# Kernel optimization log

Hardware: AMD Instinct MI355X
Metric: run time of the kernel (lower is better)

## Reference

```python
import jax, jax.numpy as jnp
import numpy as np

B, C, H, W = 8, 512, 32, 32
HEADS = 8
DIM = C // HEADS
EPS = 1e-5


def setup_inputs() -> dict:
    key = jax.random.key(0)
    ks = jax.random.split(key, 7)
    scale = 1.0 / np.sqrt(C)
    return {
        "x": jax.random.normal(ks[0], (B, C, H, W), dtype=jnp.float32),
        "gn_gamma": jnp.ones((C,), dtype=jnp.float32),
        "gn_beta": jnp.zeros((C,), dtype=jnp.float32),
        "w_qkv": jax.random.normal(ks[1], (3 * HEADS * DIM, C), dtype=jnp.float32) * scale,
        "b_qkv": jax.random.normal(ks[2], (3 * HEADS * DIM,), dtype=jnp.float32) * 0.01,
        "w_proj": jax.random.normal(ks[3], (C, HEADS * DIM), dtype=jnp.float32) * scale,
        "b_proj": jax.random.normal(ks[4], (C,), dtype=jnp.float32) * 0.01,
    }


def reference(x, gn_gamma, gn_beta, w_qkv, b_qkv, w_proj, b_proj):
    b, c, h, w = x.shape
    n = h * w
    # GroupNorm with 1 group: normalize over (C,H,W) per sample (biased var)
    mu = jnp.mean(x, axis=(1, 2, 3), keepdims=True)
    var = jnp.var(x, axis=(1, 2, 3), keepdims=True)
    xn = (x - mu) * jax.lax.rsqrt(var + EPS)
    xn = xn * gn_gamma[None, :, None, None] + gn_beta[None, :, None, None]
    # 1x1 conv QKV projection == channel matmul
    qkv = jnp.einsum('bchw,oc->bohw', xn, w_qkv) + b_qkv[None, :, None, None]
    qkv = qkv.reshape(b, 3, HEADS, DIM, n)  # matches view(B,3*heads,dim,N).chunk(3,dim=1)
    q, k, v = qkv[:, 0], qkv[:, 1], qkv[:, 2]  # each (B, heads, dim, N)
    # scale uses full channel count C, as in the source (C ** -0.5)
    dot = jnp.einsum('bhdn,bhdm->bhnm', q, k) * (c ** -0.5)
    attn = jax.nn.softmax(dot, axis=-1)
    vals = jnp.einsum('bhnm,bhdm->bhdn', attn, v)  # (B, heads, dim, N)
    vals = vals.reshape(b, HEADS * DIM, h, w)
    return jnp.einsum('bchw,oc->bohw', vals, w_proj) + b_proj[None, :, None, None]
```

## Files before the change

### kernel.cpp

```cpp
#include <hip/hip_runtime.h>
#include <hip/hip_bf16.h>
#include <math.h>

#define NB 8
#define NC 512
#define NN 1024
#define NHEADS 8
#define EPSV 1e-5f
#define SC2F 0.06376351307f

typedef __attribute__((ext_vector_type(8))) short bf16x8;
typedef __attribute__((ext_vector_type(4))) short bf16x4;
typedef __attribute__((ext_vector_type(4))) float f32x4;
typedef __attribute__((ext_vector_type(16))) float f32x16;

#define MFMA16(a,b,c) __builtin_amdgcn_mfma_f32_16x16x32_bf16(a,b,c,0,0,0)
#define MFMA32(a,b,c) __builtin_amdgcn_mfma_f32_32x32x16_bf16(a,b,c,0,0,0)

static __device__ __forceinline__ short f2bf(float f) {
    __hip_bfloat16 h = __float2bfloat16(f);
    return *reinterpret_cast<short*>(&h);
}

static __device__ __forceinline__ unsigned cvt_pk_bf16(float lo, float hi) {
    unsigned r;
    asm("v_cvt_pk_bf16_f32 %0, %1, %2" : "=v"(r) : "v"(lo), "v"(hi));
    return r;
}

static __device__ __forceinline__ void gload16(const void* g, void* l) {
    __builtin_amdgcn_global_load_lds((const __attribute__((address_space(1))) void*)g,
                                     (__attribute__((address_space(3))) void*)l, 16, 0, 0);
}

#define WS_PART_SUM 0
#define WS_PART_SQ  1024
#define WS_XNT   4096
#define WS_QT    (WS_XNT  + 2097152)
#define WS_KT    (WS_QT   + 2097152)
#define WS_V     (WS_KT   + 2097152)
#define WS_VALST (WS_V    + 2097152)
#define WS_WQB   (WS_VALST+ 2097152)
#define WS_WPB   (WS_WQB  + 393216)

__global__ __launch_bounds__(256) void prep_kernel(const float* __restrict__ x,
                                                   const float* __restrict__ wq,
                                                   const float* __restrict__ wp,
                                                   float* __restrict__ ws) {
    int blk = blockIdx.x;
    int b = blk >> 6;
    int s = blk & 63;
    const float* xb = x + (size_t)b * (NC * NN) + (size_t)s * 8192;
    float sum = 0.f, sq = 0.f;
    for (int i = threadIdx.x; i < 2048; i += 256) {
        float4 v = ((const float4*)xb)[i];
        sum += v.x + v.y + v.z + v.w;
        sq  += v.x*v.x + v.y*v.y + v.z*v.z + v.w*v.w;
    }
    #pragma unroll
    for (int off = 32; off; off >>= 1) {
        sum += __shfl_down(sum, off);
        sq  += __shfl_down(sq,  off);
    }
    __shared__ float s1[4], s2[4];
    int wave = threadIdx.x >> 6, lane = threadIdx.x & 63;
    if (lane == 0) { s1[wave] = sum; s2[wave] = sq; }

    #pragma unroll
    for (int r = 0; r < 2; r++) {
        int i = blk * 512 + threadIdx.x * 2 + r;
        const float* src;
        __hip_bfloat16* d;
        if (i < 196608) { src = wq; d = (__hip_bfloat16*)(ws + WS_WQB); }
        else            { src = wp; d = (__hip_bfloat16*)(ws + WS_WPB); i -= 196608; }
        float4 v = ((const float4*)src)[i];
        bf16x4 w;
        w[0] = f2bf(v.x); w[1] = f2bf(v.y); w[2] = f2bf(v.z); w[3] = f2bf(v.w);
        *(bf16x4*)(d + (size_t)i*4) = w;
    }

    __syncthreads();
    if (threadIdx.x == 0) {
        float a = 0.f, c2 = 0.f;
        #pragma unroll
        for (int w = 0; w < 4; w++) { a += s1[w]; c2 += s2[w]; }
        ws[WS_PART_SUM + b*64 + s] = a;
        ws[WS_PART_SQ  + b*64 + s] = c2;
    }
}

__global__ __launch_bounds__(256) void normalize_t(const float* __restrict__ x,
                                                   const float* __restrict__ gamma,
                                                   const float* __restrict__ beta,
                                                   const float* __restrict__ ws,
                                                   __hip_bfloat16* __restrict__ xnT) {
    int nt = blockIdx.x & 15, ct = (blockIdx.x >> 4) & 7, b = blockIdx.x >> 7;
    __shared__ __hip_bfloat16 tb[64][72];
    float s = 0.f, q = 0.f;
    const float4* ps = (const float4*)(ws + WS_PART_SUM + b*64);
    const float4* pq = (const float4*)(ws + WS_PART_SQ  + b*64);
    #pragma unroll
    for (int i = 0; i < 16; i++) {
        float4 a = ps[i]; s += a.x + a.y + a.z + a.w;
        float4 c = pq[i]; q += c.x + c.y + c.z + c.w;
    }
    const float inv = 1.f / (float)(NC * NN);
    float mu   = s * inv;
    float var  = q * inv - mu * mu;
    float rstd = rsqrtf(var + EPSV);

    const float* xb = x + ((size_t)b*512 + ct*64)*1024 + nt*64;
    int t = threadIdx.x;
    int cl = t >> 4, n4 = (t & 15) * 4;
    #pragma unroll
    for (int i = 0; i < 4; i++) {
        int c = i*16 + cl;
        float gm = gamma[ct*64 + c];
        float g = gm * rstd;
        float be = beta[ct*64 + c] - mu * g;
        float4 v = *(const float4*)(xb + (size_t)c*1024 + n4);
        tb[n4+0][c] = __float2bfloat16(v.x*g + be);
        tb[n4+1][c] = __float2bfloat16(v.y*g + be);
        tb[n4+2][c] = __float2bfloat16(v.z*g + be);
        tb[n4+3][c] = __float2bfloat16(v.w*g + be);
    }
    __syncthreads();
    #pragma unroll
    for (int i = 0; i < 2; i++) {
        int idx = i*256 + t;
        int n = idx >> 3, c8 = (idx & 7) * 8;
        *(bf16x8*)(xnT + ((size_t)b*1024 + nt*64 + n)*512 + ct*64 + c8) =
            *(const bf16x8*)&tb[n][c8];
    }
}

template<int OT, int MODE>
__global__ __launch_bounds__(256) void gemm_mfma(const __hip_bfloat16* __restrict__ Aw,
                                                 const __hip_bfloat16* __restrict__ Bx,
                                                 const float* __restrict__ bias,
                                                 float* __restrict__ Yout,
                                                 __hip_bfloat16* __restrict__ QTx,
                                                 __hip_bfloat16* __restrict__ KTx,
                                                 __hip_bfloat16* __restrict__ Vx) {
    __shared__ __align__(16) __hip_bfloat16 lds_raw[17408];
    const int bx = blockIdx.x;
    const int swz = (bx & 7) * (OT * 8) + (bx >> 3);
    const int nt = swz & 7;
    const int ot = (swz >> 3) % OT;
    const int bb = swz / (8 * OT);
    const int o0 = ot * 128, n0 = nt * 128;

    const int t = threadIdx.x, wv = t >> 6, l = t & 63;
    const int lr = l & 31, lh = l >> 5;
    const int wr = wv >> 1, wc = wv & 1;

    const __hip_bfloat16* Ag = Aw + (size_t)o0 * 512;
    const __hip_bfloat16* Bg = Bx + ((size_t)bb * 1024 + n0) * 512;
    __hip_bfloat16* Ab = lds_raw;
    __hip_bfloat16* Bb = lds_raw + 128*64;

    f32x16 acc[2][2];
    #pragma unroll
    for (int a1 = 0; a1 < 2; a1++)
        #pragma unroll
        for (int a2 = 0; a2 < 2; a2++)
            #pragma unroll
            for (int r = 0; r < 16; r++) acc[a1][a2][r] = 0.f;

    const int srow = wv*8 + (l >> 3);
    const int sblk = (l & 7) ^ (l >> 3);

    for (int k0 = 0; k0 < 512; k0 += 64) {
        __syncthreads();
        #pragma unroll
        for (int c = 0; c < 4; c++) {
            int row = c*32 + srow;
            gload16(Ag + (size_t)row*512 + k0 + sblk*8, Ab + (c*32 + wv*8)*64);
            gload16(Bg + (size_t)row*512 + k0 + sblk*8, Bb + (c*32 + wv*8)*64);
        }
        __syncthreads();
        #pragma unroll
        for (int ks = 0; ks < 4; ks++) {
            bf16x8 af[2], bfr[2];
            #pragma unroll
            for (int mi = 0; mi < 2; mi++) {
                int row = wr*64 + mi*32 + lr;
                af[mi] = *(const bf16x8*)(Ab + row*64 + (((ks*2 + lh) ^ (row & 7)) * 8));
            }
            #pragma unroll
            for (int ni = 0; ni < 2; ni++) {
                int row = wc*64 + ni*32 + lr;
                bfr[ni] = *(const bf16x8*)(Bb + row*64 + (((ks*2 + lh) ^ (row & 7)) * 8));
            }
            acc[0][0] = MFMA32(af[0], bfr[0], acc[0][0]);
            acc[0][1] = MFMA32(af[0], bfr[1], acc[0][1]);
            acc[1][0] = MFMA32(af[1], bfr[0], acc[1][0]);
            acc[1][1] = MFMA32(af[1], bfr[1], acc[1][1]);
        }
    }

    if (MODE == 0) {
        #pragma unroll
        for (int mi = 0; mi < 2; mi++)
            #pragma unroll
            for (int q = 0; q < 4; q++) {
                int obase = o0 + wr*64 + mi*32 + 8*q + 4*lh;
                float4 bv = *(const float4*)(bias + obase);
                #pragma unroll
                for (int ni = 0; ni < 2; ni++) {
                    int nn = n0 + wc*64 + ni*32 + lr;
                    #pragma unroll
                    for (int j = 0; j < 4; j++)
                        Yout[((size_t)bb*512 + obase + j)*1024 + nn] = acc[mi][ni][q*4+j] + bv[j];
                }
            }
    } else {
        int sec = o0 >> 9;
        if (sec == 2) {
            int od0 = o0 & 511;
            int mperm = ((lr & 12) << 1) + ((lr & 16) >> 2) + (lr & 3);
            #pragma unroll
            for (int mi = 0; mi < 2; mi++)
                #pragma unroll
                for (int q = 0; q < 4; q++) {
                    int ob = wr*64 + mi*32 + 8*q + 4*lh;
                    float4 bv = *(const float4*)(bias + o0 + ob);
                    #pragma unroll
                    for (int j = 0; j < 4; j++) {
                        int ol = od0 + ob + j;
                        int h = ol >> 6, d = ol & 63;
                        __hip_bfloat16* dst = Vx + ((size_t)((bb<<3) + h)*64 + d)*1024;
                        #pragma unroll
                        for (int ni = 0; ni < 2; ni++) {
                            int nn = n0 + wc*64 + ni*32 + mperm;
                            dst[nn] = __float2bfloat16(acc[mi][ni][q*4+j] + bv[j]);
                        }
                    }
                }
        } else {
            const float qs = (sec == 0) ? SC2F : 1.0f;
            __syncthreads();
            __hip_bfloat16* tb = lds_raw;
            #pragma unroll
            for (int mi = 0; mi < 2; mi++)
                #pragma unroll
                for (int q = 0; q < 4; q++) {
                    int ob = wr*64 + mi*32 + 8*q + 4*lh;
                    float4 bv = *(const float4*)(bias + o0 + ob);
                    #pragma unroll
                    for (int ni = 0; ni < 2; ni++) {
                        int nn = wc*64 + ni*32 + lr;
                        bf16x4 w;
                        #pragma unroll
                        for (int j = 0; j < 4; j++) w[j] = f2bf((acc[mi][ni][q*4+j] + bv[j]) * qs);
                        *(bf16x4*)&tb[(size_t)nn*136 + ob] = w;
                    }
                }
            __syncthreads();
            __hip_bfloat16* dst0 = (sec == 0) ? QTx : KTx;
            int h0 = (o0 & 511) >> 6;
            #pragma unroll
            for (int i = 0; i < 8; i++) {
                int idx = i*256 + t;
                int n = idx >> 4, rem = idx & 15;
                int hh = rem >> 3, slot = rem & 7;
                int hf32 = (slot & 4) << 3;
                int g4   = (slot & 3) << 2;
                bf16x4 lo = *(const bf16x4*)&tb[(size_t)n*136 + hh*64 + hf32 + g4];
                bf16x4 hi = *(const bf16x4*)&tb[(size_t)n*136 + hh*64 + hf32 + 16 + g4];
                bf16x8 w;
                w[0]=lo[0]; w[1]=lo[1]; w[2]=lo[2]; w[3]=lo[3];
                w[4]=hi[0]; w[5]=hi[1]; w[6]=hi[2]; w[7]=hi[3];
                *(bf16x8*)(dst0 + ((size_t)((bb<<3) + h0 + hh)*1024 + n0 + n)*64 + slot*8) = w;
            }
        }
    }
}

__global__ __launch_bounds__(512) void attn_mfma(const __hip_bfloat16* __restrict__ QT,
                                                 const __hip_bfloat16* __restrict__ KT,
                                                 const __hip_bfloat16* __restrict__ Vb,
                                                 __hip_bfloat16* __restrict__ valsT) {
    const int bh = ((blockIdx.x & 7) << 3) | ((blockIdx.x >> 3) & 7);
    const int qt = blockIdx.x >> 6;
    const int t = threadIdx.x;
    const int wv = t >> 6, lane = t & 63;
    const int g = lane >> 4, li = lane & 15;

    const __hip_bfloat16* QTg = QT + (size_t)bh * NN * 64;
    const __hip_bfloat16* KTg = KT + (size_t)bh * NN * 64;
    const __hip_bfloat16* Vg  = Vb + (size_t)bh * 64 * NN;

    __shared__ __align__(16) __hip_bfloat16 k_ls[3*4096];
    __shared__ __align__(16) __hip_bfloat16 v_ls[3*4096];

    const int nq0 = qt*128 + wv*16;

    bf16x8 qf[2];
    {
        const __hip_bfloat16* qp = QTg + (size_t)(nq0 + li) * 64;
        qf[0] = *(const bf16x8*)(qp + 8*g);
        qf[1] = *(const bf16x8*)(qp + 32 + 8*g);
    }

    bf16x8 onesf;
    #pragma unroll
    for (int j = 0; j < 8; j++) onesf[j] = (short)0x3F80;

    float m_run = 0.0f;
    f32x4 o_acc[4], o_l;
    #pragma unroll
    for (int dt = 0; dt < 4; dt++) { o_acc[dt][0]=0.f; o_acc[dt][1]=0.f; o_acc[dt][2]=0.f; o_acc[dt][3]=0.f; }
    o_l[0]=0.f; o_l[1]=0.f; o_l[2]=0.f; o_l[3]=0.f;

    auto STAGE = [&](int buf, int ck) {
        const int mc0 = ck * 64;
        int row = t >> 3, sl = t & 7;
        int sk = sl ^ (row & 7);
        gload16(KTg + (size_t)(mc0+row)*64 + sk*8, k_ls + buf*4096 + t*8);
        gload16(Vg + (size_t)row*NN + mc0 + sk*8, v_ls + buf*4096 + t*8);
    };

    STAGE(0, 0);
    STAGE(1, 1);
    asm volatile("s_waitcnt vmcnt(2)" ::: "memory");
    __builtin_amdgcn_s_barrier();

    for (int ck = 0; ck < 16; ck++) {
        const int cb = ck % 3;
        if (ck < 14) STAGE((ck + 2) % 3, ck + 2);

        const __hip_bfloat16* kb = k_ls + cb*4096;
        const __hip_bfloat16* vb = v_ls + cb*4096;

        f32x4 cini;
        cini[0] = -m_run; cini[1] = -m_run; cini[2] = -m_run; cini[3] = -m_run;
        f32x4 s_acc[4];
        __builtin_amdgcn_s_setprio(1);
        #pragma unroll
        for (int mt = 0; mt < 4; mt++) {
            f32x4 c = cini;
            #pragma unroll
            for (int hf = 0; hf < 2; hf++) {
                int row = mt*16 + li;
                int sl = ((hf<<2) + g) ^ (li & 7);
                bf16x8 kf = *(const bf16x8*)(kb + row*64 + sl*8);
                c = MFMA16(kf, qf[hf], c);
            }
            s_acc[mt] = c;
        }
        __builtin_amdgcn_s_setprio(0);

        float cmax = fmaxf(s_acc[0][0], s_acc[0][1]);
        cmax = fmaxf(fmaxf(cmax, s_acc[0][2]), s_acc[0][3]);
        cmax = fmaxf(fmaxf(cmax, s_acc[1][0]), s_acc[1][1]);
        cmax = fmaxf(fmaxf(cmax, s_acc[1][2]), s_acc[1][3]);
        cmax = fmaxf(fmaxf(cmax, s_acc[2][0]), s_acc[2][1]);
        cmax = fmaxf(fmaxf(cmax, s_acc[2][2]), s_acc[2][3]);
        cmax = fmaxf(fmaxf(cmax, s_acc[3][0]), s_acc[3][1]);
        cmax = fmaxf(fmaxf(cmax, s_acc[3][2]), s_acc[3][3]);
        cmax = fmaxf(cmax, __shfl_xor(cmax, 16));
        cmax = fmaxf(cmax, __shfl_xor(cmax, 32));

        if (ck == 0) {
            #pragma unroll
            for (int mt = 0; mt < 4; mt++) {
                s_acc[mt][0] -= cmax; s_acc[mt][1] -= cmax;
                s_acc[mt][2] -= cmax; s_acc[mt][3] -= cmax;
            }
            m_run = cmax;
        } else if (!__all(cmax <= 8.0f)) {
            float d = fmaxf(cmax, 0.0f);
            float resc = __builtin_amdgcn_exp2f(-d);
            f32x4 rv;
            #pragma unroll
            for (int r = 0; r < 4; r++) rv[r] = __shfl(resc, 4*g + r);
            #pragma unroll
            for (int dt = 0; dt < 4; dt++) {
                o_acc[dt][0]*=rv[0]; o_acc[dt][1]*=rv[1]; o_acc[dt][2]*=rv[2]; o_acc[dt][3]*=rv[3];
            }
            o_l[0]*=rv[0]; o_l[1]*=rv[1]; o_l[2]*=rv[2]; o_l[3]*=rv[3];
            #pragma unroll
            for (int mt = 0; mt < 4; mt++) {
                s_acc[mt][0] -= d; s_acc[mt][1] -= d;
                s_acc[mt][2] -= d; s_acc[mt][3] -= d;
            }
            m_run += d;
        }

        bf16x8 pf[2];
        #pragma unroll
        for (int ks = 0; ks < 2; ks++) {
            union { bf16x8 v; unsigned u[4]; } pk;
            #pragma unroll
            for (int d4 = 0; d4 < 4; d4++) {
                const int i0 = 8*ks + 2*d4, i1 = i0 + 1;
                float e0 = __builtin_amdgcn_exp2f(s_acc[i0>>2][i0&3]);
                float e1 = __builtin_amdgcn_exp2f(s_acc[i1>>2][i1&3]);
                pk.u[d4] = cvt_pk_bf16(e0, e1);
            }
            pf[ks] = pk.v;
        }

        __builtin_amdgcn_s_setprio(1);
        #pragma unroll
        for (int dt = 0; dt < 4; dt++) {
            #pragma unroll
            for (int ks = 0; ks < 2; ks++) {
                int row = dt*16 + li;
                int sl = ((ks<<2) + g) ^ (li & 7);
                bf16x8 vf = *(const bf16x8*)(vb + row*64 + sl*8);
                o_acc[dt] = MFMA16(pf[ks], vf, o_acc[dt]);
            }
        }
        o_l = MFMA16(pf[0], onesf, o_l);
        o_l = MFMA16(pf[1], onesf, o_l);
        __builtin_amdgcn_s_setprio(0);

        if (ck < 14) asm volatile("s_waitcnt vmcnt(2)" ::: "memory");
        else         asm volatile("s_waitcnt vmcnt(0)" ::: "memory");
        __builtin_amdgcn_s_barrier();
    }

    f32x4 lv;
    #pragma unroll
    for (int r = 0; r < 4; r++) lv[r] = 1.0f / o_l[r];
    const int bI = bh >> 3, hI = bh & 7;
    __hip_bfloat16* vt = valsT + (size_t)bI*1024*512 + hI*64;
    #pragma unroll
    for (int dt = 0; dt < 4; dt++)
        #pragma unroll
        for (int r = 0; r < 4; r++)
            vt[(size_t)(nq0 + 4*g + r)*512 + dt*16 + li] = __float2bfloat16(o_acc[dt][r]*lv[r]);
}

extern "C" void kernel_launch(void* const* d_in, const int* in_sizes, int n_in,
                              void* d_out, int out_size, void* d_ws, size_t ws_size,
                              hipStream_t stream) {
    const float* x      = (const float*)d_in[0];
    const float* gamma  = (const float*)d_in[1];
    const float* beta   = (const float*)d_in[2];
    const float* w_qkv  = (const float*)d_in[3];
    const float* b_qkv  = (const float*)d_in[4];
    const float* w_proj = (const float*)d_in[5];
    const float* b_proj = (const float*)d_in[6];
    float* ws   = (float*)d_ws;
    float* out  = (float*)d_out;
    __hip_bfloat16* xnT   = (__hip_bfloat16*)(ws + WS_XNT);
    __hip_bfloat16* QT    = (__hip_bfloat16*)(ws + WS_QT);
    __hip_bfloat16* KT    = (__hip_bfloat16*)(ws + WS_KT);
    __hip_bfloat16* Vx    = (__hip_bfloat16*)(ws + WS_V);
    __hip_bfloat16* valsT = (__hip_bfloat16*)(ws + WS_VALST);
    __hip_bfloat16* wqb   = (__hip_bfloat16*)(ws + WS_WQB);
    __hip_bfloat16* wpb   = (__hip_bfloat16*)(ws + WS_WPB);

    prep_kernel<<<dim3(512), dim3(256), 0, stream>>>(x, w_qkv, w_proj, ws);
    normalize_t<<<dim3(1024), dim3(256), 0, stream>>>(x, gamma, beta, ws, xnT);
    gemm_mfma<12, 1><<<dim3(768), dim3(256), 0, stream>>>(wqb, xnT, b_qkv,
                                                          nullptr, QT, KT, Vx);
    attn_mfma<<<dim3(512), dim3(512), 0, stream>>>(QT, KT, Vx, valsT);
    gemm_mfma<4, 0><<<dim3(256), dim3(256), 0, stream>>>(wpb, valsT, b_proj,
                                                         out, nullptr, nullptr, nullptr);
}
```

Before: 74.14 us.

## Process two query tiles per wave in attention, halving block size

The attention kernel now runs 4 waves per block instead of 8, with each wave handling 32 query rows (two 16-row groups) instead of 16. Each K and V fragment read from LDS feeds two MFMAs, halving LDS read traffic per unit of compute, and each thread issues two staging loads per buffer with the vmcnt waits adjusted. The cost is more registers per thread (doubled accumulators and softmax state) and fewer waves per block to hide latency.

```diff
diff --git a/kernel.cpp b/kernel.cpp
--- a/kernel.cpp
+++ b/kernel.cpp
@@ -277,7 +277,7 @@
     }
 }
 
-__global__ __launch_bounds__(512) void attn_mfma(const __hip_bfloat16* __restrict__ QT,
+__global__ __launch_bounds__(256) void attn_mfma(const __hip_bfloat16* __restrict__ QT,
                                                  const __hip_bfloat16* __restrict__ KT,
                                                  const __hip_bfloat16* __restrict__ Vb,
                                                  __hip_bfloat16* __restrict__ valsT) {
@@ -294,36 +294,44 @@
     __shared__ __align__(16) __hip_bfloat16 k_ls[3*4096];
     __shared__ __align__(16) __hip_bfloat16 v_ls[3*4096];
 
-    const int nq0 = qt*128 + wv*16;
-
-    bf16x8 qf[2];
-    {
-        const __hip_bfloat16* qp = QTg + (size_t)(nq0 + li) * 64;
-        qf[0] = *(const bf16x8*)(qp + 8*g);
-        qf[1] = *(const bf16x8*)(qp + 32 + 8*g);
+    const int nq0 = qt*128 + wv*32;
+
+    bf16x8 qf[2][2];
+    #pragma unroll
+    for (int go = 0; go < 2; go++) {
+        const __hip_bfloat16* qp = QTg + (size_t)(nq0 + go*16 + li) * 64;
+        qf[go][0] = *(const bf16x8*)(qp + 8*g);
+        qf[go][1] = *(const bf16x8*)(qp + 32 + 8*g);
     }
 
     bf16x8 onesf;
     #pragma unroll
     for (int j = 0; j < 8; j++) onesf[j] = (short)0x3F80;
 
-    float m_run = 0.0f;
-    f32x4 o_acc[4], o_l;
-    #pragma unroll
-    for (int dt = 0; dt < 4; dt++) { o_acc[dt][0]=0.f; o_acc[dt][1]=0.f; o_acc[dt][2]=0.f; o_acc[dt][3]=0.f; }
-    o_l[0]=0.f; o_l[1]=0.f; o_l[2]=0.f; o_l[3]=0.f;
+    float m_run[2] = {0.0f, 0.0f};
+    f32x4 o_acc[2][4], o_l[2];
+    #pragma unroll
+    for (int go = 0; go < 2; go++) {
+        #pragma unroll
+        for (int dt = 0; dt < 4; dt++) { o_acc[go][dt][0]=0.f; o_acc[go][dt][1]=0.f; o_acc[go][dt][2]=0.f; o_acc[go][dt][3]=0.f; }
+        o_l[go][0]=0.f; o_l[go][1]=0.f; o_l[go][2]=0.f; o_l[go][3]=0.f;
+    }
 
     auto STAGE = [&](int buf, int ck) {
         const int mc0 = ck * 64;
-        int row = t >> 3, sl = t & 7;
-        int sk = sl ^ (row & 7);
-        gload16(KTg + (size_t)(mc0+row)*64 + sk*8, k_ls + buf*4096 + t*8);
-        gload16(Vg + (size_t)row*NN + mc0 + sk*8, v_ls + buf*4096 + t*8);
+        #pragma unroll
+        for (int p = 0; p < 2; p++) {
+            int idx = t + p*256;
+            int row = idx >> 3, sl = idx & 7;
+            int sk = sl ^ (row & 7);
+            gload16(KTg + (size_t)(mc0+row)*64 + sk*8, k_ls + buf*4096 + idx*8);
+            gload16(Vg + (size_t)row*NN + mc0 + sk*8, v_ls + buf*4096 + idx*8);
+        }
     };
 
     STAGE(0, 0);
     STAGE(1, 1);
-    asm volatile("s_waitcnt vmcnt(2)" ::: "memory");
+    asm volatile("s_waitcnt vmcnt(4)" ::: "memory");
     __builtin_amdgcn_s_barrier();
 
     for (int ck = 0; ck < 16; ck++) {
@@ -333,73 +341,91 @@
         const __hip_bfloat16* kb = k_ls + cb*4096;
         const __hip_bfloat16* vb = v_ls + cb*4096;
 
-        f32x4 cini;
-        cini[0] = -m_run; cini[1] = -m_run; cini[2] = -m_run; cini[3] = -m_run;
-        f32x4 s_acc[4];
+        f32x4 s_acc[2][4];
+        f32x4 cini0, cini1;
+        cini0[0] = -m_run[0]; cini0[1] = -m_run[0]; cini0[2] = -m_run[0]; cini0[3] = -m_run[0];
+        cini1[0] = -m_run[1]; cini1[1] = -m_run[1]; cini1[2] = -m_run[1]; cini1[3] = -m_run[1];
         __builtin_amdgcn_s_setprio(1);
         #pragma unroll
         for (int mt = 0; mt < 4; mt++) {
-            f32x4 c = cini;
+            f32x4 c0 = cini0, c1 = cini1;
             #pragma unroll
             for (int hf = 0; hf < 2; hf++) {
                 int row = mt*16 + li;
                 int sl = ((hf<<2) + g) ^ (li & 7);
                 bf16x8 kf = *(const bf16x8*)(kb + row*64 + sl*8);
-                c = MFMA16(kf, qf[hf], c);
-            }
-            s_acc[mt] = c;
+                c0 = MFMA16(kf, qf[0][hf], c0);
+                c1 = MFMA16(kf, qf[1][hf], c1);
+            }
+            s_acc[0][mt] = c0;
+            s_acc[1][mt] = c1;
         }
         __builtin_amdgcn_s_setprio(0);
 
-        float cmax = fmaxf(s_acc[0][0], s_acc[0][1]);
-        cmax = fmaxf(fmaxf(cmax, s_acc[0][2]), s_acc[0][3]);
-        cmax = fmaxf(fmaxf(cmax, s_acc[1][0]), s_acc[1][1]);
-        cmax = fmaxf(fmaxf(cmax, s_acc[1][2]), s_acc[1][3]);
-        cmax = fmaxf(fmaxf(cmax, s_acc[2][0]), s_acc[2][1]);
-        cmax = fmaxf(fmaxf(cmax, s_acc[2][2]), s_acc[2][3]);
-        cmax = fmaxf(fmaxf(cmax, s_acc[3][0]), s_acc[3][1]);
-        cmax = fmaxf(fmaxf(cmax, s_acc[3][2]), s_acc[3][3]);
-        cmax = fmaxf(cmax, __shfl_xor(cmax, 16));
-        cmax = fmaxf(cmax, __shfl_xor(cmax, 32));
+        float cmax[2];
+        #pragma unroll
+        for (int go = 0; go < 2; go++) {
+            float cm = fmaxf(s_acc[go][0][0], s_acc[go][0][1]);
+            cm = fmaxf(fmaxf(cm, s_acc[go][0][2]), s_acc[go][0][3]);
+            cm = fmaxf(fmaxf(cm, s_acc[go][1][0]), s_acc[go][1][1]);
+            cm = fmaxf(fmaxf(cm, s_acc[go][1][2]), s_acc[go][1][3]);
+            cm = fmaxf(fmaxf(cm, s_acc[go][2][0]), s_acc[go][2][1]);
+            cm = fmaxf(fmaxf(cm, s_acc[go][2][2]), s_acc[go][2][3]);
+            cm = fmaxf(fmaxf(cm, s_acc[go][3][0]), s_acc[go][3][1]);
+            cm = fmaxf(fmaxf(cm, s_acc[go][3][2]), s_acc[go][3][3]);
+            cm = fmaxf(cm, __shfl_xor(cm, 16));
+            cm = fmaxf(cm, __shfl_xor(cm, 32));
+            cmax[go] = cm;
+        }
 
         if (ck == 0) {
             #pragma unroll
-            for (int mt = 0; mt < 4; mt++) {
-                s_acc[mt][0] -= cmax; s_acc[mt][1] -= cmax;
-                s_acc[mt][2] -= cmax; s_acc[mt][3] -= cmax;
-            }
-            m_run = cmax;
-        } else if (!__all(cmax <= 8.0f)) {
-            float d = fmaxf(cmax, 0.0f);
-            float resc = __builtin_amdgcn_exp2f(-d);
-            f32x4 rv;
-            #pragma unroll
-            for (int r = 0; r < 4; r++) rv[r] = __shfl(resc, 4*g + r);
-            #pragma unroll
-            for (int dt = 0; dt < 4; dt++) {
-                o_acc[dt][0]*=rv[0]; o_acc[dt][1]*=rv[1]; o_acc[dt][2]*=rv[2]; o_acc[dt][3]*=rv[3];
-            }
-            o_l[0]*=rv[0]; o_l[1]*=rv[1]; o_l[2]*=rv[2]; o_l[3]*=rv[3];
-            #pragma unroll
-            for (int mt = 0; mt < 4; mt++) {
-                s_acc[mt][0] -= d; s_acc[mt][1] -= d;
-                s_acc[mt][2] -= d; s_acc[mt][3] -= d;
-            }
-            m_run += d;
-        }
-
-        bf16x8 pf[2];
-        #pragma unroll
-        for (int ks = 0; ks < 2; ks++) {
-            union { bf16x8 v; unsigned u[4]; } pk;
-            #pragma unroll
-            for (int d4 = 0; d4 < 4; d4++) {
-                const int i0 = 8*ks + 2*d4, i1 = i0 + 1;
-                float e0 = __builtin_amdgcn_exp2f(s_acc[i0>>2][i0&3]);
-                float e1 = __builtin_amdgcn_exp2f(s_acc[i1>>2][i1&3]);
-                pk.u[d4] = cvt_pk_bf16(e0, e1);
-            }
-            pf[ks] = pk.v;
+            for (int go = 0; go < 2; go++) {
+                #pragma unroll
+                for (int mt = 0; mt < 4; mt++) {
+                    s_acc[go][mt][0] -= cmax[go]; s_acc[go][mt][1] -= cmax[go];
+                    s_acc[go][mt][2] -= cmax[go]; s_acc[go][mt][3] -= cmax[go];
+                }
+                m_run[go] = cmax[go];
+            }
+        } else if (!__all(cmax[0] <= 8.0f && cmax[1] <= 8.0f)) {
+            #pragma unroll
+            for (int go = 0; go < 2; go++) {
+                float d = fmaxf(cmax[go], 0.0f);
+                float resc = __builtin_amdgcn_exp2f(-d);
+                f32x4 rv;
+                #pragma unroll
+                for (int r = 0; r < 4; r++) rv[r] = __shfl(resc, 4*g + r);
+                #pragma unroll
+                for (int dt = 0; dt < 4; dt++) {
+                    o_acc[go][dt][0]*=rv[0]; o_acc[go][dt][1]*=rv[1];
+                    o_acc[go][dt][2]*=rv[2]; o_acc[go][dt][3]*=rv[3];
+                }
+                o_l[go][0]*=rv[0]; o_l[go][1]*=rv[1]; o_l[go][2]*=rv[2]; o_l[go][3]*=rv[3];
+                #pragma unroll
+                for (int mt = 0; mt < 4; mt++) {
+                    s_acc[go][mt][0] -= d; s_acc[go][mt][1] -= d;
+                    s_acc[go][mt][2] -= d; s_acc[go][mt][3] -= d;
+                }
+                m_run[go] += d;
+            }
+        }
+
+        bf16x8 pf[2][2];
+        #pragma unroll
+        for (int go = 0; go < 2; go++) {
+            #pragma unroll
+            for (int ks = 0; ks < 2; ks++) {
+                union { bf16x8 v; unsigned u[4]; } pk;
+                #pragma unroll
+                for (int d4 = 0; d4 < 4; d4++) {
+                    const int i0 = 8*ks + 2*d4, i1 = i0 + 1;
+                    float e0 = __builtin_amdgcn_exp2f(s_acc[go][i0>>2][i0&3]);
+                    float e1 = __builtin_amdgcn_exp2f(s_acc[go][i1>>2][i1&3]);
+                    pk.u[d4] = cvt_pk_bf16(e0, e1);
+                }
+                pf[go][ks] = pk.v;
+            }
         }
 
         __builtin_amdgcn_s_setprio(1);
@@ -410,28 +436,36 @@
                 int row = dt*16 + li;
                 int sl = ((ks<<2) + g) ^ (li & 7);
                 bf16x8 vf = *(const bf16x8*)(vb + row*64 + sl*8);
-                o_acc[dt] = MFMA16(pf[ks], vf, o_acc[dt]);
-            }
-        }
-        o_l = MFMA16(pf[0], onesf, o_l);
-        o_l = MFMA16(pf[1], onesf, o_l);
+                o_acc[0][dt] = MFMA16(pf[0][ks], vf, o_acc[0][dt]);
+                o_acc[1][dt] = MFMA16(pf[1][ks], vf, o_acc[1][dt]);
+            }
+        }
+        #pragma unroll
+        for (int go = 0; go < 2; go++) {
+            o_l[go] = MFMA16(pf[go][0], onesf, o_l[go]);
+            o_l[go] = MFMA16(pf[go][1], onesf, o_l[go]);
+        }
         __builtin_amdgcn_s_setprio(0);
 
-        if (ck < 14) asm volatile("s_waitcnt vmcnt(2)" ::: "memory");
+        if (ck < 14) asm volatile("s_waitcnt vmcnt(4)" ::: "memory");
         else         asm volatile("s_waitcnt vmcnt(0)" ::: "memory");
         __builtin_amdgcn_s_barrier();
     }
 
-    f32x4 lv;
-    #pragma unroll
-    for (int r = 0; r < 4; r++) lv[r] = 1.0f / o_l[r];
     const int bI = bh >> 3, hI = bh & 7;
     __hip_bfloat16* vt = valsT + (size_t)bI*1024*512 + hI*64;
     #pragma unroll
-    for (int dt = 0; dt < 4; dt++)
-        #pragma unroll
-        for (int r = 0; r < 4; r++)
-            vt[(size_t)(nq0 + 4*g + r)*512 + dt*16 + li] = __float2bfloat16(o_acc[dt][r]*lv[r]);
+    for (int go = 0; go < 2; go++) {
+        f32x4 lv;
+        #pragma unroll
+        for (int r = 0; r < 4; r++) lv[r] = 1.0f / o_l[go][r];
+        #pragma unroll
+        for (int dt = 0; dt < 4; dt++)
+            #pragma unroll
+            for (int r = 0; r < 4; r++)
+                vt[(size_t)(nq0 + go*16 + 4*g + r)*512 + dt*16 + li] =
+                    __float2bfloat16(o_acc[go][dt][r]*lv[r]);
+    }
 }
 
 extern "C" void kernel_launch(void* const* d_in, const int* in_sizes, int n_in,
@@ -458,7 +492,7 @@
     normalize_t<<<dim3(1024), dim3(256), 0, stream>>>(x, gamma, beta, ws, xnT);
     gemm_mfma<12, 1><<<dim3(768), dim3(256), 0, stream>>>(wqb, xnT, b_qkv,
                                                           nullptr, QT, KT, Vx);
-    attn_mfma<<<dim3(512), dim3(512), 0, stream>>>(QT, KT, Vx, valsT);
+    attn_mfma<<<dim3(512), dim3(256), 0, stream>>>(QT, KT, Vx, valsT);
     gemm_mfma<4, 0><<<dim3(256), dim3(256), 0, stream>>>(wpb, valsT, b_proj,
                                                          out, nullptr, nullptr, nullptr);
 }
```

Measured after the change: 79.55 us. 7.3% more time.
